# Performance work log

Hardware: AMD Instinct MI355X
Metric: run time of the kernel (lower is better)

## Reference

```python
import jax, jax.numpy as jnp
import numpy as np

P = 7          # output_size
SCALE = 0.125  # spatial_scale
S = 2          # sampling_ratio


def setup_inputs() -> dict:
    key = jax.random.key(0)
    k1, k2, k3, k4, k5, k6 = jax.random.split(key, 6)
    N, C, H, W, R = 8, 256, 100, 100, 512
    x = jax.random.normal(k1, (N, C, H, W), dtype=jnp.float32)
    b = jax.random.randint(k2, (R,), 0, N).astype(jnp.float32)
    x1 = jax.random.uniform(k3, (R,)) * 600.0
    y1 = jax.random.uniform(k4, (R,)) * 600.0
    bw = 10.0 + jax.random.uniform(k5, (R,)) * 190.0
    bh = 10.0 + jax.random.uniform(k6, (R,)) * 190.0
    rois = jnp.stack([b, x1, y1, x1 + bw, y1 + bh], axis=1).astype(jnp.float32)
    return {"x": x, "rois": rois}


def _axis_terms(c, L):
    # Per-axis bilinear terms, matching torchvision bilinear_interpolate.
    valid = (c > -1.0) & (c < L)          # whole sample zeroed if out of range
    c = jnp.clip(c, 0.0, L - 1.0)          # low clamp at 0; >=L-1 -> frac 0
    lo = jnp.minimum(jnp.floor(c).astype(jnp.int32), L - 1)
    hi = jnp.minimum(lo + 1, L - 1)
    frac = c - lo.astype(c.dtype)
    w_lo = jnp.where(valid, 1.0 - frac, 0.0)
    w_hi = jnp.where(valid, frac, 0.0)
    return lo, hi, w_lo, w_hi


def roi_align(x, rois):
    # aligned=True RoIAlign. x: [N,C,H,W], rois: [R,5] -> [R,C,P,P]
    N, C, H, W = x.shape
    b = rois[:, 0].astype(jnp.int32)
    sx = rois[:, 1] * SCALE - 0.5
    sy = rois[:, 2] * SCALE - 0.5
    bin_w = (rois[:, 3] * SCALE - 0.5 - sx) / P
    bin_h = (rois[:, 4] * SCALE - 0.5 - sy) / P

    frac = (jnp.arange(S, dtype=x.dtype) + 0.5) / S   # sample offset within bin
    bins = jnp.arange(P, dtype=x.dtype)
    grid = bins[None, :, None] + frac[None, None, :]   # [1,P,S]
    ys = sy[:, None, None] + grid * bin_h[:, None, None]  # [R,P,S]
    xs = sx[:, None, None] + grid * bin_w[:, None, None]  # [R,P,S]

    yl, yh, wy1, wy2 = _axis_terms(ys, H)
    xl, xh, wx1, wx2 = _axis_terms(xs, W)

    bb = b[:, None, None, None, None]
    Yl, Yh = yl[:, :, :, None, None], yh[:, :, :, None, None]  # [R,P,S,1,1]
    Xl, Xh = xl[:, None, None, :, :], xh[:, None, None, :, :]  # [R,1,1,P,S]

    def g(Y, X):
        # gather -> [R,Py,Sy,Px,Sx,C]
        return x[bb, :, Y, X]

    def w(wy, wx):
        return (wy[:, :, :, None, None] * wx[:, None, None, :, :])[..., None]

    val = (g(Yl, Xl) * w(wy1, wx1) + g(Yl, Xh) * w(wy1, wx2)
           + g(Yh, Xl) * w(wy2, wx1) + g(Yh, Xh) * w(wy2, wx2))
    # average over the SxS sampling grid per bin
    out = val.sum(axis=(2, 4)) / float(S * S)   # [R,Py,Px,C]
    return jnp.transpose(out, (0, 3, 1, 2))      # [R,C,P,P]


def reference(x, rois):
    return roi_align(x, rois)
```

## Files before the change

### kernel.cpp

```cpp
#include <hip/hip_runtime.h>

#define POOL 7
#define CCH 256
#define GCH 4
#define HH 100
#define WW 100
#define HW (HH * WW)
#define MAXTH 28
#define NTAP 14
#define RECI 128
#define NT 256

static constexpr float SCALE = 0.125f;

__device__ __attribute__((aligned(16))) int g_rec[1024 * RECI];

__device__ __forceinline__ void tap_calc(float s0, float step, int k, int L,
                                         int& lo, int& hi, float& w1, float& w2)
{
    const int   p  = k >> 1, si = k & 1;
    const float g  = (float)p + ((float)si + 0.5f) * 0.5f;
    const float c  = s0 + g * step;
    const float Lf = (float)L;
    const bool  valid = (c > -1.0f) && (c < Lf);
    float cl = fminf(fmaxf(c, 0.0f), Lf - 1.0f);
    lo = (int)floorf(cl);
    if (lo > L - 1) lo = L - 1;
    hi = lo + 1;
    if (hi > L - 1) hi = L - 1;
    const float fr = cl - (float)lo;
    w1 = valid ? 1.0f - fr : 0.0f;
    w2 = valid ? fr : 0.0f;
}

__global__ __launch_bounds__(64) void roi_pre(const float* __restrict__ rois,
                                              int* __restrict__ rec, int R)
{
    const int r = blockIdx.x;
    if (r >= R) return;
    int* rr = (rec ? rec : g_rec) + r * RECI;
    const int t = threadIdx.x;

    const float sx0 = rois[r * 5 + 1] * SCALE - 0.5f;
    const float sy0 = rois[r * 5 + 2] * SCALE - 0.5f;
    const float bw  = (rois[r * 5 + 3] * SCALE - 0.5f - sx0) * (1.0f / POOL);
    const float bh  = (rois[r * 5 + 4] * SCALE - 0.5f - sy0) * (1.0f / POOL);

    if (t < 2 * NTAP) {
        const int   axis = (t >= NTAP) ? 1 : 0;
        const int   k    = axis ? t - NTAP : t;
        const float s0   = axis ? sy0 : sx0;
        const float st   = axis ? bh : bw;
        const int   L    = axis ? HH : WW;
        int lo, hi, lo0, u0; float w1, w2, ua, ub;
        tap_calc(s0, st, k, L, lo, hi, w1, w2);
        tap_calc(s0, st, 0, L, lo0, u0, ua, ub);
        const int base = axis ? lo0 : (lo0 & ~3);
        int* tp = rr + 8 + (axis ? 4 * NTAP : 0) + k * 4;
        tp[0] = max(lo - base, 0);
        tp[1] = max(hi - base, 0);
        tp[2] = __float_as_int(w1);
        tp[3] = __float_as_int(w2);
    } else if (t == 2 * NTAP) {
        int xl0, xh0, xl13, xh13, yl0, yh0, yl13, yh13; float a, b;
        tap_calc(sx0, bw, 0,        WW, xl0,  xh0,  a, b);
        tap_calc(sx0, bw, NTAP - 1, WW, xl13, xh13, a, b);
        tap_calc(sy0, bh, 0,        HH, yl0,  yh0,  a, b);
        tap_calc(sy0, bh, NTAP - 1, HH, yl13, yh13, a, b);
        const int xmin_al = xl0 & ~3;
        int TH  = yh13 - yl0 + 1; if (TH > MAXTH) TH = MAXTH;
        int nb4 = (xh13 - xmin_al) / 4 + 1;
        if (nb4 > 8) nb4 = 8;
        rr[0] = (int)rois[r * 5 + 0];
        rr[1] = xmin_al;
        rr[2] = yl0;
        rr[3] = TH;
        rr[4] = nb4;
        rr[5] = (65536 + nb4 - 1) / nb4;
    }
}

__global__ __launch_bounds__(NT, 8) void roi_main(
    const float* __restrict__ x, const int* __restrict__ rec_in,
    float* __restrict__ out)
{
    __shared__ float tile[GCH * MAXTH * 32];
    __shared__ int   s_tap[2 * NTAP * 4];

    const int bid = blockIdx.x;
    const int r   = bid >> 6;
    const int c0  = (bid & 63) * GCH;
    const int t   = threadIdx.x;

    const int* rr = (rec_in ? rec_in : g_rec) + r * RECI;
    const int n       = rr[0];
    const int xmin_al = rr[1];
    const int ymin    = rr[2];
    const int TH      = rr[3];
    const int nb4     = rr[4];
    const int magic   = rr[5];

    if (t < 2 * NTAP) {
        __builtin_amdgcn_global_load_lds(
            (const __attribute__((address_space(1))) void*)(rr + 8 + t * 4),
            (__attribute__((address_space(3))) void*)(s_tap + t * 4),
            16, 0, 0);
    }

    const int chstride = TH * (nb4 << 2);
    const int tot      = TH * nb4;

    {
        const int ch   = t >> 6;
        const int lane = t & 63;
        const float* xb = x + ((size_t)(n * CCH + c0 + ch)) * HW
                            + (size_t)ymin * WW + xmin_al;
        float* lbase = tile + ch * chstride;
        for (int idx = lane; idx < tot; idx += 64) {
            const int row = (idx * magic) >> 16;
            const int b   = idx - row * nb4;
            __builtin_amdgcn_global_load_lds(
                (const __attribute__((address_space(1))) void*)(xb + row * WW + (b << 2)),
                (__attribute__((address_space(3))) void*)(lbase + (idx << 2)),
                16, 0, 0);
        }
    }
    __syncthreads();

    const int ch  = t >> 6;
    const int bin = t & 63;
    if (bin < POOL * POOL) {
        const int py = bin / POOL;
        const int px = bin - py * POOL;
        const int TWp = nb4 << 2;
        const float* tc = tile + ch * chstride;
        float acc = 0.0f;
        #pragma unroll
        for (int sy = 0; sy < 2; ++sy) {
            const int* yt = s_tap + 4 * NTAP + (py * 2 + sy) * 4;
            const int   rowl = yt[0] * TWp;
            const int   rowh = yt[1] * TWp;
            const float wy1 = __int_as_float(yt[2]);
            const float wy2 = __int_as_float(yt[3]);
            #pragma unroll
            for (int sx = 0; sx < 2; ++sx) {
                const int* xt = s_tap + (px * 2 + sx) * 4;
                const int   xl  = xt[0], xh = xt[1];
                const float wx1 = __int_as_float(xt[2]);
                const float wx2 = __int_as_float(xt[3]);
                acc += wy1 * (wx1 * tc[rowl + xl] + wx2 * tc[rowl + xh])
                     + wy2 * (wx1 * tc[rowh + xl] + wx2 * tc[rowh + xh]);
            }
        }
        out[(size_t)(r * CCH + c0 + ch) * (POOL * POOL) + bin] = acc * 0.25f;
    }
}

extern "C" void kernel_launch(void* const* d_in, const int* in_sizes, int n_in,
                              void* d_out, int out_size, void* d_ws, size_t ws_size,
                              hipStream_t stream) {
    const float* x    = (const float*)d_in[0];
    const float* rois = (const float*)d_in[1];
    float*       out  = (float*)d_out;

    const int R = in_sizes[1] / 5;
    int* rec = (ws_size >= (size_t)R * RECI * sizeof(int)) ? (int*)d_ws : nullptr;

    roi_pre<<<R, 64, 0, stream>>>(rois, rec, R);
    roi_main<<<R * (CCH / GCH), NT, 0, stream>>>(x, rec, out);
}
```

Baseline: 41.79 us.

## Pipeline per-wave channel loop with double-buffered async LDS loads

Each wave now handles 16 consecutive channels of one ROI rather than one block handling 4 channels. It double-buffers global-to-LDS loads and uses explicit vmcnt waits, so loading the next channel overlaps with interpolating the current one, and no block-wide barrier is needed. Sample offsets and weights are precomputed in registers once per wave. Block indices are also swizzled across groups of 8. The aim is to hide memory latency and cut the cost of syncs and per-block setup, at the price of fewer, longer waves, higher register use and more hand-written waitcnt code.

```diff
diff --git a/kernel.cpp b/kernel.cpp
--- a/kernel.cpp
+++ b/kernel.cpp
@@ -2,7 +2,6 @@
 
 #define POOL 7
 #define CCH 256
-#define GCH 4
 #define HH 100
 #define WW 100
 #define HW (HH * WW)
@@ -10,6 +9,8 @@
 #define NTAP 14
 #define RECI 128
 #define NT 256
+#define ITEMS 16
+#define SLOTF 1024
 
 static constexpr float SCALE = 0.125f;
 
@@ -80,17 +81,103 @@
     }
 }
 
-__global__ __launch_bounds__(NT, 8) void roi_main(
+template <int NJ>
+__device__ __forceinline__ void run_items(
+    const float* __restrict__ x, float* __restrict__ out,
+    float* wslot, const int* __restrict__ rr,
+    int n, int c0, int r, int xmin_al, int ymin,
+    int TWp, int tot, int magic, int nb4, int lane)
+{
+    const int bin = (lane < POOL * POOL) ? lane : POOL * POOL - 1;
+    const int py  = bin / POOL;
+    const int px  = bin - py * POOL;
+
+    const int4* tp = (const int4*)(rr + 8);
+    const int4 xt0 = tp[px * 2],        xt1 = tp[px * 2 + 1];
+    const int4 yt0 = tp[NTAP + py * 2], yt1 = tp[NTAP + py * 2 + 1];
+
+    int   off[16];
+    float wgt[16];
+    #pragma unroll
+    for (int s = 0; s < 4; ++s) {
+        const int4 xt = (s & 1) ? xt1 : xt0;
+        const int4 yt = (s >> 1) ? yt1 : yt0;
+        const int   bl  = yt.x * TWp, bh = yt.y * TWp;
+        const float wy1 = __int_as_float(yt.z), wy2 = __int_as_float(yt.w);
+        const float wx1 = __int_as_float(xt.z), wx2 = __int_as_float(xt.w);
+        off[s * 4 + 0] = bl + xt.x;  wgt[s * 4 + 0] = wy1 * wx1;
+        off[s * 4 + 1] = bl + xt.y;  wgt[s * 4 + 1] = wy1 * wx2;
+        off[s * 4 + 2] = bh + xt.x;  wgt[s * 4 + 2] = wy2 * wx1;
+        off[s * 4 + 3] = bh + xt.y;  wgt[s * 4 + 3] = wy2 * wx2;
+    }
+
+    int soff[NJ];
+    #pragma unroll
+    for (int j = 0; j < NJ; ++j) {
+        int idx = lane + 64 * j;
+        if (idx >= tot) idx = tot - 1;
+        const int row = (idx * magic) >> 16;
+        const int b   = idx - row * nb4;
+        soff[j] = row * WW + (b << 2);
+    }
+
+    const float* xb    = x + ((size_t)(n * CCH + c0)) * HW
+                           + (size_t)ymin * WW + xmin_al;
+    float*       obase = out + ((size_t)(r * CCH + c0)) * (POOL * POOL) + bin;
+
+    #pragma unroll
+    for (int j = 0; j < NJ; ++j)
+        __builtin_amdgcn_global_load_lds(
+            (const __attribute__((address_space(1))) void*)(xb + soff[j]),
+            (__attribute__((address_space(3))) void*)(wslot + j * 256),
+            16, 0, 0);
+
+    #pragma unroll
+    for (int k = 0; k < ITEMS; ++k) {
+        if (k + 1 < ITEMS) {
+            const float* xk  = xb + (size_t)(k + 1) * HW;
+            float*       dst = wslot + ((k + 1) & 1) * SLOTF;
+            #pragma unroll
+            for (int j = 0; j < NJ; ++j)
+                __builtin_amdgcn_global_load_lds(
+                    (const __attribute__((address_space(1))) void*)(xk + soff[j]),
+                    (__attribute__((address_space(3))) void*)(dst + j * 256),
+                    16, 0, 0);
+            if constexpr (NJ == 1)      asm volatile("s_waitcnt vmcnt(1)" ::: "memory");
+            else if constexpr (NJ == 2) asm volatile("s_waitcnt vmcnt(2)" ::: "memory");
+            else if constexpr (NJ == 3) asm volatile("s_waitcnt vmcnt(3)" ::: "memory");
+            else                        asm volatile("s_waitcnt vmcnt(4)" ::: "memory");
+        } else {
+            asm volatile("s_waitcnt vmcnt(0)" ::: "memory");
+        }
+        const float* buf = wslot + (k & 1) * SLOTF;
+        float a0 = 0.f, a1 = 0.f, a2 = 0.f, a3 = 0.f;
+        #pragma unroll
+        for (int i = 0; i < 16; i += 4) {
+            a0 += wgt[i + 0] * buf[off[i + 0]];
+            a1 += wgt[i + 1] * buf[off[i + 1]];
+            a2 += wgt[i + 2] * buf[off[i + 2]];
+            a3 += wgt[i + 3] * buf[off[i + 3]];
+        }
+        if (lane < POOL * POOL)
+            obase[k * (POOL * POOL)] = (a0 + a1 + a2 + a3) * 0.25f;
+    }
+}
+
+__global__ __launch_bounds__(NT) void roi_main(
     const float* __restrict__ x, const int* __restrict__ rec_in,
-    float* __restrict__ out)
-{
-    __shared__ float tile[GCH * MAXTH * 32];
-    __shared__ int   s_tap[2 * NTAP * 4];
-
-    const int bid = blockIdx.x;
-    const int r   = bid >> 6;
-    const int c0  = (bid & 63) * GCH;
-    const int t   = threadIdx.x;
+    float* __restrict__ out, int nblocks)
+{
+    __shared__ float tile[(NT / 64) * 2 * SLOTF];
+
+    const int bid  = blockIdx.x;
+    const int swb  = ((nblocks & 7) == 0)
+                   ? ((bid & 7) * (nblocks >> 3) + (bid >> 3)) : bid;
+    const int wib  = threadIdx.x >> 6;
+    const int lane = threadIdx.x & 63;
+    const int wave = swb * (NT / 64) + wib;
+    const int r    = wave >> 4;
+    const int c0   = (wave & 15) * ITEMS;
 
     const int* rr = (rec_in ? rec_in : g_rec) + r * RECI;
     const int n       = rr[0];
@@ -99,60 +186,17 @@
     const int TH      = rr[3];
     const int nb4     = rr[4];
     const int magic   = rr[5];
-
-    if (t < 2 * NTAP) {
-        __builtin_amdgcn_global_load_lds(
-            (const __attribute__((address_space(1))) void*)(rr + 8 + t * 4),
-            (__attribute__((address_space(3))) void*)(s_tap + t * 4),
-            16, 0, 0);
-    }
-
-    const int chstride = TH * (nb4 << 2);
-    const int tot      = TH * nb4;
-
-    {
-        const int ch   = t >> 6;
-        const int lane = t & 63;
-        const float* xb = x + ((size_t)(n * CCH + c0 + ch)) * HW
-                            + (size_t)ymin * WW + xmin_al;
-        float* lbase = tile + ch * chstride;
-        for (int idx = lane; idx < tot; idx += 64) {
-            const int row = (idx * magic) >> 16;
-            const int b   = idx - row * nb4;
-            __builtin_amdgcn_global_load_lds(
-                (const __attribute__((address_space(1))) void*)(xb + row * WW + (b << 2)),
-                (__attribute__((address_space(3))) void*)(lbase + (idx << 2)),
-                16, 0, 0);
-        }
-    }
-    __syncthreads();
-
-    const int ch  = t >> 6;
-    const int bin = t & 63;
-    if (bin < POOL * POOL) {
-        const int py = bin / POOL;
-        const int px = bin - py * POOL;
-        const int TWp = nb4 << 2;
-        const float* tc = tile + ch * chstride;
-        float acc = 0.0f;
-        #pragma unroll
-        for (int sy = 0; sy < 2; ++sy) {
-            const int* yt = s_tap + 4 * NTAP + (py * 2 + sy) * 4;
-            const int   rowl = yt[0] * TWp;
-            const int   rowh = yt[1] * TWp;
-            const float wy1 = __int_as_float(yt[2]);
-            const float wy2 = __int_as_float(yt[3]);
-            #pragma unroll
-            for (int sx = 0; sx < 2; ++sx) {
-                const int* xt = s_tap + (px * 2 + sx) * 4;
-                const int   xl  = xt[0], xh = xt[1];
-                const float wx1 = __int_as_float(xt[2]);
-                const float wx2 = __int_as_float(xt[3]);
-                acc += wy1 * (wx1 * tc[rowl + xl] + wx2 * tc[rowl + xh])
-                     + wy2 * (wx1 * tc[rowh + xl] + wx2 * tc[rowh + xh]);
-            }
-        }
-        out[(size_t)(r * CCH + c0 + ch) * (POOL * POOL) + bin] = acc * 0.25f;
+    const int tot     = TH * nb4;
+    const int TWp     = nb4 << 2;
+    const int nj      = (tot + 63) >> 6;
+
+    float* wslot = tile + wib * (2 * SLOTF);
+
+    switch (nj) {
+    case 1:  run_items<1>(x, out, wslot, rr, n, c0, r, xmin_al, ymin, TWp, tot, magic, nb4, lane); break;
+    case 2:  run_items<2>(x, out, wslot, rr, n, c0, r, xmin_al, ymin, TWp, tot, magic, nb4, lane); break;
+    case 3:  run_items<3>(x, out, wslot, rr, n, c0, r, xmin_al, ymin, TWp, tot, magic, nb4, lane); break;
+    default: run_items<4>(x, out, wslot, rr, n, c0, r, xmin_al, ymin, TWp, tot, magic, nb4, lane); break;
     }
 }
 
@@ -166,6 +210,9 @@
     const int R = in_sizes[1] / 5;
     int* rec = (ws_size >= (size_t)R * RECI * sizeof(int)) ? (int*)d_ws : nullptr;
 
+    const int waves   = R * (CCH / ITEMS);
+    const int nblocks = waves / (NT / 64);
+
     roi_pre<<<R, 64, 0, stream>>>(rois, rec, R);
-    roi_main<<<R * (CCH / GCH), NT, 0, stream>>>(x, rec, out);
-}
+    roi_main<<<nblocks, NT, 0, stream>>>(x, rec, out, nblocks);
+}
```

New measurement: 58.13 us. 1.39x slower.
